# Kernel tuning notes

Measured on AMD Instinct MI355X. Metric: run time of the kernel, lower is better.

Reference implementation:

```python
import jax, jax.numpy as jnp
import numpy as np

FRAME_SIZE = 160

def _gru(x, h0, wih, whh, bih, bhh):
    # x: [B,T,D], h0: [B,U]; torch GRU gate order: r, z, n
    xp = jnp.einsum('btd,gd->btg', x, wih) + bih  # [B,T,3U]
    def step(h, xt):
        hp = h @ whh.T + bhh
        xr, xz, xn = jnp.split(xt, 3, axis=-1)
        hr, hz, hn = jnp.split(hp, 3, axis=-1)
        r = jax.nn.sigmoid(xr + hr)
        z = jax.nn.sigmoid(xz + hz)
        n = jnp.tanh(xn + r * hn)
        h_new = (1.0 - z) * n + z * h
        return h_new, h_new
    hT, ys = jax.lax.scan(step, h0, jnp.swapaxes(xp, 0, 1))
    return jnp.swapaxes(ys, 0, 1), hT

def _conv1d(x, w, b):
    # x: [B,C,T], w: [O,I,K], valid padding
    y = jax.lax.conv_general_dilated(x, w, (1,), 'VALID', dimension_numbers=('NCH', 'OIH', 'NCH'))
    return y + b[None, :, None]

def setup_inputs() -> dict:
    key = jax.random.key(0)
    ks = jax.random.split(key, 24)
    B, T, FD = 16, 36, 20
    PE, CD, K = 64, 128, 3
    SE, UA, UB, OUT = 128, 384, 64, 256
    NS = 3
    S = (T - 2 * (K - 1)) * FRAME_SIZE  # 32 * 160 = 5120
    s = 0.05
    inp = {
        'features': jax.random.normal(ks[0], (B, T, FD), jnp.float32),
        'periods': jax.random.randint(ks[1], (B, T, 1), 0, 256),
        'signals': jax.random.randint(ks[2], (B, S, NS), 0, 256),
        'gru_a_state': jnp.zeros((B, UA), jnp.float32),
        'gru_b_state': jnp.zeros((B, UB), jnp.float32),
        'period_emb': jax.random.normal(ks[3], (256, PE), jnp.float32) * s,
        'signal_emb': jax.random.normal(ks[4], (256, SE), jnp.float32) * s,
        'conv1_w': jax.random.normal(ks[5], (CD, FD + PE, K), jnp.float32) * s,
        'conv1_b': jnp.zeros((CD,), jnp.float32),
        'conv2_w': jax.random.normal(ks[6], (CD, CD, K), jnp.float32) * s,
        'conv2_b': jnp.zeros((CD,), jnp.float32),
        'fd1_w': jax.random.normal(ks[7], (CD, CD), jnp.float32) * s,
        'fd1_b': jnp.zeros((CD,), jnp.float32),
        'fd2_w': jax.random.normal(ks[8], (CD, CD), jnp.float32) * s,
        'fd2_b': jnp.zeros((CD,), jnp.float32),
        'grua_wih': jax.random.normal(ks[9], (3 * UA, NS * SE + CD), jnp.float32) * s,
        'grua_whh': jax.random.normal(ks[10], (3 * UA, UA), jnp.float32) * s,
        'grua_bih': jnp.zeros((3 * UA,), jnp.float32),
        'grua_bhh': jnp.zeros((3 * UA,), jnp.float32),
        'grub_wih': jax.random.normal(ks[11], (3 * UB, UA + CD), jnp.float32) * s,
        'grub_whh': jax.random.normal(ks[12], (3 * UB, UB), jnp.float32) * s,
        'grub_bih': jnp.zeros((3 * UB,), jnp.float32),
        'grub_bhh': jnp.zeros((3 * UB,), jnp.float32),
        'fc1_w': jax.random.normal(ks[13], (OUT, UB), jnp.float32) * s,
        'fc1_b': jnp.zeros((OUT,), jnp.float32),
        'fc2_w': jax.random.normal(ks[14], (OUT, UB), jnp.float32) * s,
        'fc2_b': jnp.zeros((OUT,), jnp.float32),
        'alpha': jnp.ones((OUT,), jnp.float32),
        'beta': jnp.ones((OUT,), jnp.float32),
    }
    return inp

def reference(features, periods, signals, gru_a_state, gru_b_state, period_emb,
              signal_emb, conv1_w, conv1_b, conv2_w, conv2_b, fd1_w, fd1_b,
              fd2_w, fd2_b, grua_wih, grua_whh, grua_bih, grua_bhh, grub_wih,
              grub_whh, grub_bih, grub_bhh, fc1_w, fc1_b, fc2_w, fc2_b, alpha, beta):
    B = features.shape[0]
    # ---- frame rate network ----
    ep = period_emb[periods].reshape(B, periods.shape[1], -1)  # [B,T,PE]
    f = jnp.concatenate([features, ep], axis=-1)               # [B,T,FD+PE]
    c = jnp.transpose(f, (0, 2, 1))                            # [B,C,T]
    c = jnp.tanh(_conv1d(c, conv1_w, conv1_b))
    c = jnp.tanh(_conv1d(c, conv2_w, conv2_b))
    c = jnp.transpose(c, (0, 2, 1))                            # [B,T-4,CD]
    c = jnp.tanh(c @ fd1_w.T + fd1_b)
    c = jnp.tanh(c @ fd2_w.T + fd2_b)
    # ---- sample rate network ----
    es = signal_emb[signals].reshape(B, signals.shape[1], -1)  # [B,S,NS*SE]
    c_up = jnp.repeat(c, FRAME_SIZE, axis=1)                   # [B,S,CD]
    y = jnp.concatenate([es, c_up], axis=-1)
    y, _ = _gru(y, gru_a_state, grua_wih, grua_whh, grua_bih, grua_bhh)
    y = jnp.concatenate([y, c_up], axis=-1)
    y, _ = _gru(y, gru_b_state, grub_wih, grub_whh, grub_bih, grub_bhh)
    # dual FC: alpha*tanh(W1 y + b1) + beta*tanh(W2 y + b2)
    y = alpha * jnp.tanh(y @ fc1_w.T + fc1_b) + beta * jnp.tanh(y @ fc2_w.T + fc2_b)
    return jax.nn.log_softmax(y, axis=-1)
```

## Files before the change

kernel.cpp:

```cpp
#include <hip/hip_runtime.h>

typedef unsigned short u16;
typedef unsigned int u32;
typedef unsigned long long u64;
typedef __attribute__((ext_vector_type(8))) short bf16x8;
typedef __attribute__((ext_vector_type(4))) float f32x4;

#define S_LEN 5120
#define UB 64
#define GA 1152
#define CAPP (1 << 16)
#define FASTCAP 3000
#define RING_WORDS (16 * 8 * 3 * 128)

__device__ __forceinline__ float bf2f(u16 u) { return __uint_as_float(((u32)u) << 16); }
__device__ __forceinline__ u16 f2bf(float f) {
    u32 x = __float_as_uint(f);
    return (u16)((x + 0x7fffu + ((x >> 16) & 1u)) >> 16);
}
__device__ __forceinline__ float blo(u32 w) { return __uint_as_float(w << 16); }
__device__ __forceinline__ float bhi(u32 w) { return __uint_as_float(w & 0xffff0000u); }
__device__ __forceinline__ float sigm(float x) { return 1.f / (1.f + __expf(-x)); }
__device__ __forceinline__ float tanh_(float x) { float e = __expf(2.f * x); return 1.f - 2.f / (e + 1.f); }

#if __has_builtin(__builtin_amdgcn_fdot2)
typedef _Float16 h2v __attribute__((ext_vector_type(2)));
__device__ __forceinline__ float dot2p(u32 w, u32 h, float acc) {
    return __builtin_amdgcn_fdot2(__builtin_bit_cast(h2v, w), __builtin_bit_cast(h2v, h), acc, false);
}
__device__ __forceinline__ u32 packpair(float a, float b) {
    u16 x = __builtin_bit_cast(u16, (_Float16)a);
    u16 y = __builtin_bit_cast(u16, (_Float16)b);
    return (u32)x | ((u32)y << 16);
}
__device__ __forceinline__ u16 pack1(float a) { return __builtin_bit_cast(u16, (_Float16)a); }
#else
__device__ __forceinline__ float dot2p(u32 w, u32 h, float acc) {
    acc = fmaf(blo(w), blo(h), acc);
    return fmaf(bhi(w), bhi(h), acc);
}
__device__ __forceinline__ u32 packpair(float a, float b) { return (u32)f2bf(a) | ((u32)f2bf(b) << 16); }
__device__ __forceinline__ u16 pack1(float a) { return f2bf(a); }
#endif

__device__ __forceinline__ u64 ald64(const u64* p) {
    return __hip_atomic_load(p, __ATOMIC_RELAXED, __HIP_MEMORY_SCOPE_AGENT);
}
__device__ __forceinline__ u32 ald32(const u32* p) {
    return __hip_atomic_load(p, __ATOMIC_RELAXED, __HIP_MEMORY_SCOPE_AGENT);
}
__device__ __forceinline__ void ast32(u32* p, u32 v) {
    __hip_atomic_store(p, v, __ATOMIC_RELAXED, __HIP_MEMORY_SCOPE_AGENT);
}
__device__ __forceinline__ u64 ld64_sc0(const u64* p) {
    u64 v;
    asm volatile("global_load_dwordx2 %0, %1, off sc0\n\ts_waitcnt vmcnt(0)"
                 : "=v"(v) : "v"(p) : "memory");
    return v;
}
__device__ __forceinline__ void st32_sc0(u32* p, u32 v) {
    asm volatile("global_store_dword %0, %1, off sc0" :: "v"(p), "v"(v) : "memory");
}
__device__ __forceinline__ void pub32(u32* fastp, u32* slowp, u32 v) {
    st32_sc0(fastp, v);
    ast32(slowp, v);
}
__device__ __forceinline__ u64 poll64(const u64* fastp, const u64* slowp, u32 tg,
                                      bool allowFast, int* fastEn, int* dead) {
    u64 v;
    if (allowFast && *fastEn) {
        for (int i = 0; i < FASTCAP; ++i) {
            v = ld64_sc0(fastp);
            if (((u32)v & 0xffffu) == tg && (((u32)(v >> 32)) & 0xffffu) == tg) return v;
        }
        *fastEn = 0;
    }
    int cnt = 0;
    for (;;) {
        v = ald64(slowp);
        if (((u32)v & 0xffffu) == tg && (((u32)(v >> 32)) & 0xffffu) == tg) return v;
        if (*dead || ++cnt > CAPP) { *dead = 1; return v; }
    }
}

__global__ __launch_bounds__(256) void k_cvt(const float* __restrict__ src, u16* __restrict__ dst) {
    int i = blockIdx.x * 256 + threadIdx.x;
    dst[i] = f2bf(src[i]);
}

__global__ __launch_bounds__(128) void k_frame1(const float* __restrict__ features, const int* __restrict__ periods,
                                                const float* __restrict__ pemb, const float* __restrict__ w,
                                                const float* __restrict__ bias, float* __restrict__ c1) {
    __shared__ float fin[3][84];
    int t = blockIdx.x, b = blockIdx.y, o = threadIdx.x;
    for (int i = threadIdx.x; i < 252; i += 128) {
        int kk = i / 84, ci = i % 84, tt = t + kk;
        float v;
        if (ci < 20) v = features[(b * 36 + tt) * 20 + ci];
        else v = pemb[periods[b * 36 + tt] * 64 + (ci - 20)];
        fin[kk][ci] = v;
    }
    __syncthreads();
    float acc = bias[o];
    for (int kk = 0; kk < 3; kk++)
        for (int ci = 0; ci < 84; ci++)
            acc = fmaf(fin[kk][ci], w[o * 252 + ci * 3 + kk], acc);
    c1[(b * 34 + t) * 128 + o] = tanh_(acc);
}

__global__ __launch_bounds__(128) void k_frame2(const float* __restrict__ c1, const float* __restrict__ w,
                                                const float* __restrict__ bias, float* __restrict__ c2) {
    __shared__ float fin[3][128];
    int t = blockIdx.x, b = blockIdx.y, o = threadIdx.x;
    for (int i = threadIdx.x; i < 384; i += 128) {
        int kk = i >> 7, ci = i & 127;
        fin[kk][ci] = c1[(b * 34 + t + kk) * 128 + ci];
    }
    __syncthreads();
    float acc = bias[o];
    for (int kk = 0; kk < 3; kk++)
        for (int ci = 0; ci < 128; ci++)
            acc = fmaf(fin[kk][ci], w[o * 384 + ci * 3 + kk], acc);
    c2[(b * 32 + t) * 128 + o] = tanh_(acc);
}

__global__ __launch_bounds__(128) void k_fd(const float* __restrict__ c2, const float* __restrict__ w1,
                                            const float* __restrict__ b1, const float* __restrict__ w2,
                                            const float* __restrict__ b2, float* __restrict__ cc) {
    __shared__ float a0[128], a1s[128];
    int t = blockIdx.x, b = blockIdx.y, o = threadIdx.x;
    a0[o] = c2[(b * 32 + t) * 128 + o];
    __syncthreads();
    float acc = b1[o];
    for (int k = 0; k < 128; k++) acc = fmaf(a0[k], w1[o * 128 + k], acc);
    a1s[o] = tanh_(acc);
    __syncthreads();
    float acc2 = b2[o];
    for (int k = 0; k < 128; k++) acc2 = fmaf(a1s[k], w2[o * 128 + k], acc2);
    cc[(b * 32 + t) * 128 + o] = tanh_(acc2);
}

__global__ __launch_bounds__(192) void k_cpart(const float* __restrict__ cc, const float* __restrict__ wihB,
                                               const float* __restrict__ bihB, float* __restrict__ cpart) {
    __shared__ float cl[128];
    int fr = blockIdx.x, b = blockIdx.y, o = threadIdx.x;
    if (o < 128) cl[o] = cc[(b * 32 + fr) * 128 + o];
    __syncthreads();
    float acc = bihB[o];
    for (int k = 0; k < 128; k++) acc = fmaf(cl[k], wihB[o * 512 + 384 + k], acc);
    cpart[((size_t)b * 32 + fr) * 192 + o] = acc;
}

__global__ __launch_bounds__(256) void k_init(u32* base, int n) {
    int i = blockIdx.x * 256 + threadIdx.x;
    if (i < n) ast32(base + i, 0u);
}

__global__ __launch_bounds__(256) void k_gemm(const int* __restrict__ signals, const float* __restrict__ semb,
                                              const float* __restrict__ c, const u16* __restrict__ wih,
                                              const float* __restrict__ bih, u16* __restrict__ xp) {
    __shared__ u16 As[64][40];
    __shared__ u16 Bs[64][40];
    int m0 = blockIdx.x * 64, n0 = blockIdx.y * 64;
    int tid = threadIdx.x;
    int r = tid >> 2, kc = tid & 3;
    int lane = tid & 63, wv = tid >> 6;
    int wr = wv >> 1, wc = wv & 1;
    int mrow = m0 + r;
    int b = mrow / S_LEN, s = mrow % S_LEN;
    const int* sigrow = signals + mrow * 3;
    const float* crow = c + ((size_t)(b * 32) + s / 160) * 128;
    f32x4 acc[2][2];
#pragma unroll
    for (int i = 0; i < 2; i++)
#pragma unroll
        for (int j = 0; j < 2; j++) { acc[i][j][0] = 0.f; acc[i][j][1] = 0.f; acc[i][j][2] = 0.f; acc[i][j][3] = 0.f; }
    for (int k0 = 0; k0 < 512; k0 += 32) {
        int k = k0 + kc * 8;
        float v[8];
        if (k < 384) {
            int idx = sigrow[k >> 7];
            const float* src = semb + idx * 128 + (k & 127);
#pragma unroll
            for (int j = 0; j < 8; j++) v[j] = src[j];
        } else {
            const float* src = crow + (k - 384);
#pragma unroll
            for (int j = 0; j < 8; j++) v[j] = src[j];
        }
        u32 pk[4];
#pragma unroll
        for (int j = 0; j < 4; j++) pk[j] = (u32)f2bf(v[2 * j]) | ((u32)f2bf(v[2 * j + 1]) << 16);
        *(uint4*)&As[r][kc * 8] = *(uint4*)pk;
        *(uint4*)&Bs[r][kc * 8] = *(const uint4*)&wih[(size_t)(n0 + r) * 512 + k];
        __syncthreads();
        bf16x8 af[2], bfr[2];
#pragma unroll
        for (int mi = 0; mi < 2; mi++) af[mi] = *(const bf16x8*)&As[wr * 32 + mi * 16 + (lane & 15)][(lane >> 4) * 8];
#pragma unroll
        for (int ni = 0; ni < 2; ni++) bfr[ni] = *(const bf16x8*)&Bs[wc * 32 + ni * 16 + (lane & 15)][(lane >> 4) * 8];
#pragma unroll
        for (int mi = 0; mi < 2; mi++)
#pragma unroll
            for (int ni = 0; ni < 2; ni++)
                acc[mi][ni] = __builtin_amdgcn_mfma_f32_16x16x32_bf16(af[mi], bfr[ni], acc[mi][ni], 0, 0, 0);
        __syncthreads();
    }
#pragma unroll
    for (int mi = 0; mi < 2; mi++)
#pragma unroll
        for (int ni = 0; ni < 2; ni++) {
            int row = m0 + wr * 32 + mi * 16 + (lane >> 4) * 4;
            int col = n0 + wc * 32 + ni * 16 + (lane & 15);
            float bias = bih[col];
#pragma unroll
            for (int i = 0; i < 4; i++)
                xp[(size_t)(row + i) * GA + col] = f2bf(acc[mi][ni][i] + bias);
        }
}

__global__ __launch_bounds__(512) void k_serial(
        const float* __restrict__ whhA, const float* __restrict__ bhhA,
        const float* __restrict__ wihB, const float* __restrict__ whhB,
        const float* __restrict__ bhhB, const u16* __restrict__ xp,
        const float* __restrict__ cpart, const float* __restrict__ h0a,
        const float* __restrict__ h0b, u32* hExF, u32* hExS, u32* bprog,
        float* __restrict__ yB) {
    const int blk = blockIdx.x, tid = threadIdx.x;
    const int b = (blk & 7) | ((blk >> 5) << 3);
    const int role = (blk >> 3) & 3;

    if (role < 3) {
        __shared__ __align__(16) u32 hbuf[2][192];
        __shared__ float red[384][5];
        __shared__ u16 xpb[2][384];
        __shared__ int lbB, deadf, fastEn;
        const int s = role;
        const int u = tid & 127, kc = tid >> 7;
        u32 w[3][64];
        if (tid < 384) {
#pragma unroll
            for (int g = 0; g < 3; g++) {
                const float* wr = whhA + ((size_t)(g * 384 + s * 128 + u)) * 384 + kc * 128;
#pragma unroll
                for (int c = 0; c < 16; c++)
#pragma unroll
                    for (int j = 0; j < 4; j++)
                        w[g][c * 4 + j] = packpair(wr[c * 8 + 2 * j], wr[c * 8 + 2 * j + 1]);
            }
        }
        if (tid < 192) hbuf[0][tid] = packpair(h0a[b * 384 + 2 * tid], h0a[b * 384 + 2 * tid + 1]);
        const int xcol = (tid >> 7) * 384 + s * 128 + (tid & 127);
        float hprA = 0, bh0 = 0, bh1 = 0, bh2 = 0;
        if (tid < 128) {
            hprA = h0a[b * 384 + s * 128 + tid];
            bh0 = bhhA[s * 128 + tid];
            bh1 = bhhA[384 + s * 128 + tid];
            bh2 = bhhA[768 + s * 128 + tid];
        }
        if (tid < 384) xpb[0][tid] = xp[((size_t)b * S_LEN) * GA + xcol];
        if (tid == 0) { lbB = 0; deadf = 0; fastEn = 1; }
        __syncthreads();

        for (int t = 0; t < S_LEN; ++t) {
            const int p = t & 1, p2 = p ^ 1;
            u16 xnext = 0;
            int lbn = -1;
            if (tid < 384) {
                if (t + 1 < S_LEN) xnext = xp[((size_t)b * S_LEN + t + 1) * GA + xcol];
                if (tid == 0) lbn = (int)ald32(bprog + b);
            } else if (t > 0) {
                const int i = tid - 384, pi = i >> 6, idx = i & 63;
                const int ps = pi + (pi >= s ? 1 : 0);
                const size_t woff = (((size_t)b * 8 + ((t - 1) & 7)) * 3 + ps) * 64 + idx;
                u64 v = poll64((const u64*)hExF + woff, (const u64*)hExS + woff,
                               (u32)t & 0xffffu, t >= 2, &fastEn, &deadf);
                hbuf[p][ps * 64 + idx] = (((u32)v) >> 16) | (((u32)(v >> 32)) & 0xffff0000u);
            }
            __syncthreads();
            if (tid < 384) {
                const uint4* hb4 = (const uint4*)&hbuf[p][0] + kc * 16;
                float a00 = 0, a01 = 0, a10 = 0, a11 = 0, a20 = 0, a21 = 0;
#pragma unroll
                for (int c = 0; c < 16; c++) {
                    uint4 hc = hb4[c];
                    a00 = dot2p(w[0][4 * c + 0], hc.x, a00); a01 = dot2p(w[0][4 * c + 1], hc.y, a01);
                    a00 = dot2p(w[0][4 * c + 2], hc.z, a00); a01 = dot2p(w[0][4 * c + 3], hc.w, a01);
                    a10 = dot2p(w[1][4 * c + 0], hc.x, a10); a11 = dot2p(w[1][4 * c + 1], hc.y, a11);
                    a10 = dot2p(w[1][4 * c + 2], hc.z, a10); a11 = dot2p(w[1][4 * c + 3], hc.w, a11);
                    a20 = dot2p(w[2][4 * c + 0], hc.x, a20); a21 = dot2p(w[2][4 * c + 1], hc.y, a21);
                    a20 = dot2p(w[2][4 * c + 2], hc.z, a20); a21 = dot2p(w[2][4 * c + 3], hc.w, a21);
                }
                red[u][kc] = a00 + a01;
                red[128 + u][kc] = a10 + a11;
                red[256 + u][kc] = a20 + a21;
                if (t + 1 < S_LEN) xpb[p2][tid] = xnext;
                if (tid == 0 && lbn >= 0) lbB = lbn;
            }
            __syncthreads();
            if (tid < 128) {
                if (t - 7 > lbB && !deadf) {
                    int cnt = 0;
                    while ((int)ald32(bprog + b) < t - 7) {
                        if (++cnt > CAPP) { deadf = 1; break; }
                    }
                }
                float pr = red[tid][0] + red[tid][1] + red[tid][2] + bh0;
                float pz = red[128 + tid][0] + red[128 + tid][1] + red[128 + tid][2] + bh1;
                float pn = red[256 + tid][0] + red[256 + tid][1] + red[256 + tid][2] + bh2;
                float rg = sigm(bf2f(xpb[p][tid]) + pr);
                float zg = sigm(bf2f(xpb[p][128 + tid]) + pz);
                float ng = tanh_(bf2f(xpb[p][256 + tid]) + rg * pn);
                float hnew = (1.f - zg) * ng + zg * hprA;
                hprA = hnew;
                u16 hb16 = pack1(hnew);
                ((u16*)&hbuf[p2][0])[s * 128 + tid] = hb16;
                const size_t poff = (((size_t)b * 8 + (t & 7)) * 3 + s) * 128 + tid;
                pub32(hExF + poff, hExS + poff, ((u32)hb16 << 16) | (u32)(t + 1));
            }
        }
    } else {
        __shared__ __align__(16) u32 hbufA[192];
        __shared__ __align__(16) u16 hbB[2][64];
        __shared__ float redy[192][3];
        __shared__ float redh[192];
        __shared__ float cpl[32][192];
        __shared__ int deadB, fastEnB;
        const int r = (tid < 192) ? tid : tid - 192;
        const int kh = (tid < 192) ? 0 : 1;
        u32 wy[96];
        if (tid < 384) {
            const float* wr = wihB + (size_t)r * 512 + kh * 192;
#pragma unroll
            for (int i = 0; i < 96; i++) wy[i] = packpair(wr[2 * i], wr[2 * i + 1]);
        }
        u32 wb0[32], wb1[32];
        if (tid >= 384 && tid < 480) {
            const int rb = (tid - 384) * 2;
            const float* w0p = whhB + (size_t)rb * 64;
            const float* w1p = whhB + (size_t)(rb + 1) * 64;
#pragma unroll
            for (int i = 0; i < 32; i++) {
                wb0[i] = packpair(w0p[2 * i], w0p[2 * i + 1]);
                wb1[i] = packpair(w1p[2 * i], w1p[2 * i + 1]);
            }
        }
        for (int i = tid; i < 32 * 192; i += 512)
            cpl[i / 192][i % 192] = cpart[((size_t)b * 32) * 192 + i];
        float bB0 = 0, bB1 = 0, bB2 = 0, hprB = 0;
        if (tid < 64) {
            bB0 = bhhB[tid]; bB1 = bhhB[64 + tid]; bB2 = bhhB[128 + tid];
            hprB = h0b[b * 64 + tid];
            hbB[0][tid] = pack1(hprB);
        }
        if (tid == 0) { deadB = 0; fastEnB = 1; }
        __syncthreads();

        for (int tb = 0; tb < S_LEN; ++tb) {
            const int p = tb & 1, p2 = p ^ 1;
            if (tid < 192) {
                const int ps = tid >> 6, idx = tid & 63;
                const size_t woff = (((size_t)b * 8 + (tb & 7)) * 3 + ps) * 64 + idx;
                u64 v = poll64((const u64*)hExF + woff, (const u64*)hExS + woff,
                               (u32)(tb + 1) & 0xffffu, tb >= 1, &fastEnB, &deadB);
                hbufA[ps * 64 + idx] = (((u32)v) >> 16) | (((u32)(v >> 32)) & 0xffff0000u);
            }
            __syncthreads();
            if (tid < 384) {
                const uint4* hb4 = (const uint4*)&hbufA[0] + kh * 24;
                float a0 = 0, a1 = 0;
#pragma unroll
                for (int c = 0; c < 24; c++) {
                    uint4 hc = hb4[c];
                    a0 = dot2p(wy[4 * c + 0], hc.x, a0); a1 = dot2p(wy[4 * c + 1], hc.y, a1);
                    a0 = dot2p(wy[4 * c + 2], hc.z, a0); a1 = dot2p(wy[4 * c + 3], hc.w, a1);
                }
                redy[r][kh] = a0 + a1;
            } else if (tid < 480) {
                const uint4* hb4 = (const uint4*)&hbB[p][0];
                float a0 = 0, b0 = 0;
#pragma unroll
                for (int q = 0; q < 8; q++) {
                    uint4 hc = hb4[q];
                    a0 = dot2p(wb0[4 * q + 0], hc.x, a0); a0 = dot2p(wb0[4 * q + 1], hc.y, a0);
                    a0 = dot2p(wb0[4 * q + 2], hc.z, a0); a0 = dot2p(wb0[4 * q + 3], hc.w, a0);
                    b0 = dot2p(wb1[4 * q + 0], hc.x, b0); b0 = dot2p(wb1[4 * q + 1], hc.y, b0);
                    b0 = dot2p(wb1[4 * q + 2], hc.z, b0); b0 = dot2p(wb1[4 * q + 3], hc.w, b0);
                }
                const int rb = (tid - 384) * 2;
                redh[rb] = a0;
                redh[rb + 1] = b0;
            }
            __syncthreads();
            if (tid < 64) {
                const int fr = tb / 160;
                float xr = redy[tid][0] + redy[tid][1] + cpl[fr][tid];
                float xz = redy[64 + tid][0] + redy[64 + tid][1] + cpl[fr][64 + tid];
                float xn = redy[128 + tid][0] + redy[128 + tid][1] + cpl[fr][128 + tid];
                float hr = redh[tid] + bB0;
                float hz = redh[64 + tid] + bB1;
                float hn = redh[128 + tid] + bB2;
                float rg = sigm(xr + hr);
                float zg = sigm(xz + hz);
                float ng = tanh_(xn + rg * hn);
                float hnew = (1.f - zg) * ng + zg * hprB;
                hprB = hnew;
                hbB[p2][tid] = pack1(hnew);
                yB[((size_t)b * S_LEN + tb) * UB + tid] = hnew;
                if (tid == 0) ast32(bprog + b, (u32)(tb + 1));
            }
        }
    }
}

__global__ __launch_bounds__(256) void k_fc(const float* __restrict__ yB, const float* __restrict__ w1,
                                            const float* __restrict__ b1, const float* __restrict__ w2,
                                            const float* __restrict__ b2, const float* __restrict__ alpha,
                                            const float* __restrict__ beta, float* __restrict__ out) {
    __shared__ float yb[4][64];
    __shared__ float vb[4][256];
    int tid = threadIdx.x;
    size_t r0 = (size_t)blockIdx.x * 4;
    { int r = tid >> 6, k = tid & 63; yb[r][k] = yB[(r0 + r) * 64 + k]; }
    __syncthreads();
    int o = tid;
    float a1[4] = {0, 0, 0, 0}, a2[4] = {0, 0, 0, 0};
    for (int k = 0; k < 64; k += 4) {
        float4 u = *(const float4*)(w1 + o * 64 + k);
        float4 v = *(const float4*)(w2 + o * 64 + k);
#pragma unroll
        for (int r = 0; r < 4; r++) {
            float y0 = yb[r][k], y1 = yb[r][k + 1], y2 = yb[r][k + 2], y3 = yb[r][k + 3];
            a1[r] = fmaf(u.x, y0, fmaf(u.y, y1, fmaf(u.z, y2, fmaf(u.w, y3, a1[r]))));
            a2[r] = fmaf(v.x, y0, fmaf(v.y, y1, fmaf(v.z, y2, fmaf(v.w, y3, a2[r]))));
        }
    }
    float al = alpha[o], be = beta[o], c1 = b1[o], c2 = b2[o];
#pragma unroll
    for (int r = 0; r < 4; r++)
        vb[r][o] = al * tanh_(a1[r] + c1) + be * tanh_(a2[r] + c2);
    __syncthreads();
    int wv = tid >> 6, l = tid & 63;
    float x0 = vb[wv][l], x1 = vb[wv][64 + l], x2 = vb[wv][128 + l], x3 = vb[wv][192 + l];
    float m = fmaxf(fmaxf(x0, x1), fmaxf(x2, x3));
#pragma unroll
    for (int off = 1; off < 64; off <<= 1) m = fmaxf(m, __shfl_xor(m, off));
    float sum = __expf(x0 - m) + __expf(x1 - m) + __expf(x2 - m) + __expf(x3 - m);
#pragma unroll
    for (int off = 1; off < 64; off <<= 1) sum += __shfl_xor(sum, off);
    float lse = m + __logf(sum);
    float* po = out + (r0 + wv) * 256;
    po[l] = x0 - lse;
    po[64 + l] = x1 - lse;
    po[128 + l] = x2 - lse;
    po[192 + l] = x3 - lse;
}

extern "C" void kernel_launch(void* const* d_in, const int* in_sizes, int n_in,
                              void* d_out, int out_size, void* d_ws, size_t ws_size,
                              hipStream_t stream) {
    const float* features = (const float*)d_in[0];
    const int* periods = (const int*)d_in[1];
    const int* signals = (const int*)d_in[2];
    const float* gruA0 = (const float*)d_in[3];
    const float* gruB0 = (const float*)d_in[4];
    const float* period_emb = (const float*)d_in[5];
    const float* signal_emb = (const float*)d_in[6];
    const float* conv1_w = (const float*)d_in[7];
    const float* conv1_b = (const float*)d_in[8];
    const float* conv2_w = (const float*)d_in[9];
    const float* conv2_b = (const float*)d_in[10];
    const float* fd1_w = (const float*)d_in[11];
    const float* fd1_b = (const float*)d_in[12];
    const float* fd2_w = (const float*)d_in[13];
    const float* fd2_b = (const float*)d_in[14];
    const float* grua_wih = (const float*)d_in[15];
    const float* grua_whh = (const float*)d_in[16];
    const float* grua_bih = (const float*)d_in[17];
    const float* grua_bhh = (const float*)d_in[18];
    const float* grub_wih = (const float*)d_in[19];
    const float* grub_whh = (const float*)d_in[20];
    const float* grub_bih = (const float*)d_in[21];
    const float* grub_bhh = (const float*)d_in[22];
    const float* fc1_w = (const float*)d_in[23];
    const float* fc1_b = (const float*)d_in[24];
    const float* fc2_w = (const float*)d_in[25];
    const float* fc2_b = (const float*)d_in[26];
    const float* alpha = (const float*)d_in[27];
    const float* beta = (const float*)d_in[28];
    float* out = (float*)d_out;

    char* ws = (char*)d_ws;
    size_t off = 0;
    auto alloc = [&](size_t bytes) { void* p = ws + off; off += (bytes + 255) & ~(size_t)255; return p; };
    u16* xp = (u16*)alloc((size_t)16 * 5120 * 1152 * 2);
    u16* wihA = (u16*)alloc((size_t)1152 * 512 * 2);
    float* c1 = (float*)alloc((size_t)16 * 34 * 128 * 4);
    float* c2 = (float*)alloc((size_t)16 * 32 * 128 * 4);
    float* cc = (float*)alloc((size_t)16 * 32 * 128 * 4);
    float* cpart = (float*)alloc((size_t)16 * 32 * 192 * 4);
    float* yB = (float*)alloc((size_t)16 * 5120 * 64 * 4);
    u32* hExF = (u32*)alloc((size_t)RING_WORDS * 4);
    u32* hExS = (u32*)alloc((size_t)(RING_WORDS + 256) * 4);
    u32* bprog = hExS + RING_WORDS;
    const int initN = 2 * RING_WORDS + 256;

    k_cvt<<<dim3(2304), dim3(256), 0, stream>>>(grua_wih, wihA);
    k_frame1<<<dim3(34, 16), dim3(128), 0, stream>>>(features, periods, period_emb, conv1_w, conv1_b, c1);
    k_frame2<<<dim3(32, 16), dim3(128), 0, stream>>>(c1, conv2_w, conv2_b, c2);
    k_fd<<<dim3(32, 16), dim3(128), 0, stream>>>(c2, fd1_w, fd1_b, fd2_w, fd2_b, cc);
    k_cpart<<<dim3(32, 16), dim3(192), 0, stream>>>(cc, grub_wih, grub_bih, cpart);
    k_init<<<dim3((initN + 255) / 256), dim3(256), 0, stream>>>(hExF, initN);
    k_gemm<<<dim3(1280, 18), dim3(256), 0, stream>>>(signals, signal_emb, cc, wihA, grua_bih, xp);
    k_serial<<<dim3(64), dim3(512), 0, stream>>>(grua_whh, grua_bhh, grub_wih, grub_whh, grub_bhh,
                                                 xp, cpart, gruA0, gruB0, hExF, hExS, bprog, yB);
    k_fc<<<dim3(20480), dim3(256), 0, stream>>>(yB, fc1_w, fc1_b, fc2_w, fc2_b, alpha, beta, out);
}
```

Baseline: 10.26 ms.

## Rebalance GRU-A per-step work across waves and use lighter workgroup barriers

Moves the per-step xp prefetch loads off the first 128 threads (which run the gate update) onto threads 128-383, samples the GRU-B progress counter only every fourth step from a different thread, and moves the backpressure spin-wait after the hidden-state computation. Replaces __syncthreads with a custom barrier that waits only on LDS/scalar counters (lgkmcnt) and pins scheduling with sched_barrier, so outstanding global loads need not drain at each barrier. In the GRU-B block, polling moves to threads 192-383 so the gate-update wave is not stalled by it. The goal is to shorten the serial critical path of each recurrent step. The risk is that the custom barrier no longer waits on vmcnt, which could expose a memory-ordering hazard if any global load result is consumed across it.

```diff
diff --git a/kernel.cpp b/kernel.cpp
--- a/kernel.cpp
+++ b/kernel.cpp
@@ -81,6 +81,12 @@
         if (((u32)v & 0xffffu) == tg && (((u32)(v >> 32)) & 0xffffu) == tg) return v;
         if (*dead || ++cnt > CAPP) { *dead = 1; return v; }
     }
+}
+__device__ __forceinline__ void wgbar() {
+    __builtin_amdgcn_sched_barrier(0);
+    asm volatile("s_waitcnt lgkmcnt(0)" ::: "memory");
+    __builtin_amdgcn_s_barrier();
+    __builtin_amdgcn_sched_barrier(0);
 }
 
 __global__ __launch_bounds__(256) void k_cvt(const float* __restrict__ src, u16* __restrict__ dst) {
@@ -250,7 +256,10 @@
             }
         }
         if (tid < 192) hbuf[0][tid] = packpair(h0a[b * 384 + 2 * tid], h0a[b * 384 + 2 * tid + 1]);
-        const int xcol = (tid >> 7) * 384 + s * 128 + (tid & 127);
+        const int j1 = tid - 128;
+        const int xcol1 = (tid >= 128 && tid < 512) ? ((j1 >> 7) * 384 + s * 128 + (j1 & 127)) : 0;
+        const int j2 = tid + 128;
+        const int xcol2 = (tid >= 128 && tid < 256) ? ((j2 >> 7) * 384 + s * 128 + (j2 & 127)) : 0;
         float hprA = 0, bh0 = 0, bh1 = 0, bh2 = 0;
         if (tid < 128) {
             hprA = h0a[b * 384 + s * 128 + tid];
@@ -258,26 +267,33 @@
             bh1 = bhhA[384 + s * 128 + tid];
             bh2 = bhhA[768 + s * 128 + tid];
         }
-        if (tid < 384) xpb[0][tid] = xp[((size_t)b * S_LEN) * GA + xcol];
+        if (tid >= 128 && tid < 384) xpb[0][j1] = xp[((size_t)b * S_LEN) * GA + xcol1];
+        if (tid >= 128 && tid < 256) xpb[0][j2] = xp[((size_t)b * S_LEN) * GA + xcol2];
         if (tid == 0) { lbB = 0; deadf = 0; fastEn = 1; }
         __syncthreads();
 
         for (int t = 0; t < S_LEN; ++t) {
             const int p = t & 1, p2 = p ^ 1;
-            u16 xnext = 0;
+            const bool hasx = (t + 1 < S_LEN);
+            u16 xq1 = 0, xq2 = 0;
             int lbn = -1;
-            if (tid < 384) {
-                if (t + 1 < S_LEN) xnext = xp[((size_t)b * S_LEN + t + 1) * GA + xcol];
-                if (tid == 0) lbn = (int)ald32(bprog + b);
-            } else if (t > 0) {
-                const int i = tid - 384, pi = i >> 6, idx = i & 63;
-                const int ps = pi + (pi >= s ? 1 : 0);
-                const size_t woff = (((size_t)b * 8 + ((t - 1) & 7)) * 3 + ps) * 64 + idx;
-                u64 v = poll64((const u64*)hExF + woff, (const u64*)hExS + woff,
-                               (u32)t & 0xffffu, t >= 2, &fastEn, &deadf);
-                hbuf[p][ps * 64 + idx] = (((u32)v) >> 16) | (((u32)(v >> 32)) & 0xffff0000u);
-            }
-            __syncthreads();
+            if (tid >= 384) {
+                if (t > 0) {
+                    const int i = tid - 384, pi = i >> 6, idx = i & 63;
+                    const int ps = pi + (pi >= s ? 1 : 0);
+                    const size_t woff = (((size_t)b * 8 + ((t - 1) & 7)) * 3 + ps) * 64 + idx;
+                    u64 v = poll64((const u64*)hExF + woff, (const u64*)hExS + woff,
+                                   (u32)t & 0xffffu, t >= 2, &fastEn, &deadf);
+                    hbuf[p][ps * 64 + idx] = (((u32)v) >> 16) | (((u32)(v >> 32)) & 0xffff0000u);
+                }
+            } else if (tid >= 128) {
+                if (hasx) {
+                    xq1 = xp[((size_t)b * S_LEN + t + 1) * GA + xcol1];
+                    if (tid < 256) xq2 = xp[((size_t)b * S_LEN + t + 1) * GA + xcol2];
+                }
+                if (tid == 383 && (t & 3) == 0) lbn = (int)ald32(bprog + b);
+            }
+            wgbar();
             if (tid < 384) {
                 const uint4* hb4 = (const uint4*)&hbuf[p][0] + kc * 16;
                 float a00 = 0, a01 = 0, a10 = 0, a11 = 0, a20 = 0, a21 = 0;
@@ -294,17 +310,14 @@
                 red[u][kc] = a00 + a01;
                 red[128 + u][kc] = a10 + a11;
                 red[256 + u][kc] = a20 + a21;
-                if (t + 1 < S_LEN) xpb[p2][tid] = xnext;
-                if (tid == 0 && lbn >= 0) lbB = lbn;
-            }
-            __syncthreads();
+            }
+            if (hasx && tid >= 128 && tid < 384) {
+                xpb[p2][j1] = xq1;
+                if (tid < 256) xpb[p2][j2] = xq2;
+            }
+            if (tid == 383 && lbn >= 0) lbB = lbn;
+            wgbar();
             if (tid < 128) {
-                if (t - 7 > lbB && !deadf) {
-                    int cnt = 0;
-                    while ((int)ald32(bprog + b) < t - 7) {
-                        if (++cnt > CAPP) { deadf = 1; break; }
-                    }
-                }
                 float pr = red[tid][0] + red[tid][1] + red[tid][2] + bh0;
                 float pz = red[128 + tid][0] + red[128 + tid][1] + red[128 + tid][2] + bh1;
                 float pn = red[256 + tid][0] + red[256 + tid][1] + red[256 + tid][2] + bh2;
@@ -315,6 +328,12 @@
                 hprA = hnew;
                 u16 hb16 = pack1(hnew);
                 ((u16*)&hbuf[p2][0])[s * 128 + tid] = hb16;
+                if (t - 7 > lbB && !deadf) {
+                    int cnt = 0;
+                    while ((int)ald32(bprog + b) < t - 7) {
+                        if (++cnt > CAPP) { deadf = 1; break; }
+                    }
+                }
                 const size_t poff = (((size_t)b * 8 + (t & 7)) * 3 + s) * 128 + tid;
                 pub32(hExF + poff, hExS + poff, ((u32)hb16 << 16) | (u32)(t + 1));
             }
@@ -358,14 +377,14 @@
 
         for (int tb = 0; tb < S_LEN; ++tb) {
             const int p = tb & 1, p2 = p ^ 1;
-            if (tid < 192) {
-                const int ps = tid >> 6, idx = tid & 63;
+            if (tid >= 192 && tid < 384) {
+                const int i = tid - 192, ps = i >> 6, idx = i & 63;
                 const size_t woff = (((size_t)b * 8 + (tb & 7)) * 3 + ps) * 64 + idx;
                 u64 v = poll64((const u64*)hExF + woff, (const u64*)hExS + woff,
                                (u32)(tb + 1) & 0xffffu, tb >= 1, &fastEnB, &deadB);
                 hbufA[ps * 64 + idx] = (((u32)v) >> 16) | (((u32)(v >> 32)) & 0xffff0000u);
             }
-            __syncthreads();
+            wgbar();
             if (tid < 384) {
                 const uint4* hb4 = (const uint4*)&hbufA[0] + kh * 24;
                 float a0 = 0, a1 = 0;
@@ -391,7 +410,7 @@
                 redh[rb] = a0;
                 redh[rb + 1] = b0;
             }
-            __syncthreads();
+            wgbar();
             if (tid < 64) {
                 const int fr = tb / 160;
                 float xr = redy[tid][0] + redy[tid][1] + cpl[fr][tid];
```

Result: no change. 10.20 ms (-0.6%).
